# Kernel optimization log

Measured on AMD Instinct MI355X. Metric: run time of the kernel, lower is better.

## Reference

```python
import jax, jax.numpy as jnp
import numpy as np
from jax import lax

B, S, D = 4, 4096, 1024
EPS = 1e-6  # flax RMSNorm default epsilon


def setup_inputs() -> dict:
    key = jax.random.key(0)
    ks = jax.random.split(key, 8)
    std = 0.01  # flax.linen.initializers.normal() default stddev
    return {
        "x": jax.random.normal(ks[0], (B, S, D), dtype=jnp.float32),
        "wq": jax.random.normal(ks[1], (D, D), dtype=jnp.float32) * std,
        "wk": jax.random.normal(ks[2], (D, D), dtype=jnp.float32) * std,
        "wv": jax.random.normal(ks[3], (D, D), dtype=jnp.float32) * std,
        "wa": jax.random.normal(ks[4], (D, 2 * D), dtype=jnp.float32) * std,
        "wg": jax.random.normal(ks[5], (D, D), dtype=jnp.float32) * std,
        "wo": jax.random.normal(ks[6], (D, D), dtype=jnp.float32) * std,
        "rms_scale": jnp.ones((D,), dtype=jnp.float32),  # RMSNorm scale param
    }


def gate_loop_operator(k, v, q, a):
    # data-dependent complex linear recurrence: h_t = a_t * h_{t-1} + k_t * v_t
    def binary_operator(e_i, e_j):
        a_i, kv_i = e_i
        a_j, kv_j = e_j
        return (a_j * a_i, a_j * kv_i + kv_j)

    kv = (k * v).astype(jnp.complex64)
    _, y = lax.associative_scan(binary_operator, (a, kv), axis=1)
    return q * jnp.real(y)


def reference(x, wq, wk, wv, wa, wg, wo, rms_scale):
    # RMSNorm (flax default: no mean subtraction, learned scale)
    xn = x * lax.rsqrt(jnp.mean(x * x, axis=-1, keepdims=True) + EPS) * rms_scale

    q = xn @ wq
    k = xn @ wk
    v = xn @ wv
    a = xn @ wa  # [B, S, 2D]
    g = xn @ wg

    a_r, a_i = jnp.split(a, 2, axis=-1)
    a_c = lax.complex(a_r, a_i)
    magnitude = jax.nn.sigmoid(jnp.abs(a_c))  # constrain |a| < 1 for stability
    phase = jnp.angle(a_c)
    a_c = magnitude * jnp.exp(1j * phase)

    y = gate_loop_operator(k, v, q, a_c)
    y = y * jax.nn.silu(g)
    return y @ wo
```

## Files before the change

kernel.cpp:

```cpp
#include <hip/hip_runtime.h>
#include <hip/hip_bf16.h>
#include <math.h>

#define BDIM 4
#define SDIM 4096
#define DDIM 1024
#define MROWS (BDIM*SDIM)
#define EPS 1e-6f
#define NCHUNK 64
#define LCHUNK 64

typedef _Float16 f16_t;
typedef _Float16 f16x4_t __attribute__((ext_vector_type(4)));
typedef _Float16 f16x8_t __attribute__((ext_vector_type(8)));
typedef float    f32x4_t __attribute__((ext_vector_type(4)));

__device__ __forceinline__ void gload16(const void* g, void* l) {
    __builtin_amdgcn_global_load_lds(
        (const __attribute__((address_space(1))) unsigned int*)g,
        (__attribute__((address_space(3))) unsigned int*)l, 16, 0, 0);
}

__global__ __launch_bounds__(256) void fill_kernel(float* __restrict__ out,
                                                   int n, float val)
{
    const int i = blockIdx.x * 256 + threadIdx.x;
    if (i < n) out[i] = val;
}

__global__ __launch_bounds__(256) void rmsnorm_kernel(
    const float* __restrict__ x, const float* __restrict__ scale,
    f16_t* __restrict__ xn)
{
    const int row = blockIdx.x;
    const int tid = threadIdx.x;
    const float4 v = reinterpret_cast<const float4*>(x + (size_t)row * DDIM)[tid];
    float ss = v.x*v.x + v.y*v.y + v.z*v.z + v.w*v.w;
    #pragma unroll
    for (int off = 32; off > 0; off >>= 1)
        ss += __shfl_down(ss, off, 64);
    __shared__ float red[4];
    if ((tid & 63) == 0) red[tid >> 6] = ss;
    __syncthreads();
    ss = red[0] + red[1] + red[2] + red[3];
    const float inv = rsqrtf(ss * (1.0f / DDIM) + EPS);
    const float4 sc = reinterpret_cast<const float4*>(scale)[tid];
    f16x4_t o;
    o.x = (f16_t)(v.x * inv * sc.x);
    o.y = (f16_t)(v.y * inv * sc.y);
    o.z = (f16_t)(v.z * inv * sc.z);
    o.w = (f16_t)(v.w * inv * sc.w);
    reinterpret_cast<f16x4_t*>(xn + (size_t)row * DDIM)[tid] = o;
}

__global__ __launch_bounds__(256) void transpose_f16_kernel(
    const float* __restrict__ W, f16_t* __restrict__ WT, int K, int N)
{
    __shared__ float t[32][33];
    const int kb = blockIdx.y * 32;
    const int nb = blockIdx.x * 32;
    const int r  = threadIdx.x >> 3;
    const int c0 = (threadIdx.x & 7) << 2;
    const float4 v = *reinterpret_cast<const float4*>(&W[(size_t)(kb + r) * N + nb + c0]);
    t[r][c0 + 0] = v.x; t[r][c0 + 1] = v.y; t[r][c0 + 2] = v.z; t[r][c0 + 3] = v.w;
    __syncthreads();
    f16x4_t o;
    o.x = (f16_t)t[c0 + 0][r];
    o.y = (f16_t)t[c0 + 1][r];
    o.z = (f16_t)t[c0 + 2][r];
    o.w = (f16_t)t[c0 + 3][r];
    *reinterpret_cast<f16x4_t*>(&WT[(size_t)(nb + r) * K + kb + c0]) = o;
}

__global__ __launch_bounds__(256) void transpose_a_kernel(
    const float* __restrict__ W, f16_t* __restrict__ WT)
{
    const int K = DDIM, N = 2 * DDIM;
    __shared__ float t[32][33];
    const int kb = blockIdx.y * 32;
    const int nb = blockIdx.x * 32;
    const int r  = threadIdx.x >> 3;
    const int c0 = (threadIdx.x & 7) << 2;
    const int base = (c0 < 16) ? ((nb >> 1) + c0) : (DDIM + (nb >> 1) + c0 - 16);
    const float4 v = *reinterpret_cast<const float4*>(&W[(size_t)(kb + r) * N + base]);
    t[r][c0 + 0] = v.x; t[r][c0 + 1] = v.y; t[r][c0 + 2] = v.z; t[r][c0 + 3] = v.w;
    __syncthreads();
    const int rr  = threadIdx.x >> 3;
    const int cc0 = (threadIdx.x & 7) << 2;
    const int ctile = (rr >> 1) + (rr & 1) * 16;
    f16x4_t o;
    o.x = (f16_t)t[cc0 + 0][ctile];
    o.y = (f16_t)t[cc0 + 1][ctile];
    o.z = (f16_t)t[cc0 + 2][ctile];
    o.w = (f16_t)t[cc0 + 3][ctile];
    *reinterpret_cast<f16x4_t*>(&WT[(size_t)(nb + rr) * K + kb + cc0]) = o;
}

template <int MODE>
__global__ __launch_bounds__(256, 2) void mfma_gemm_kernel(
    const f16_t* __restrict__ A, const f16_t* __restrict__ BT,
    void* __restrict__ Cv, void* __restrict__ Cv2, void* __restrict__ Cv3,
    int M, int N, int K)
{
    __shared__ __align__(16) f16_t As[128 * 32];
    __shared__ __align__(16) f16_t Bs[128 * 32];

    const int tid  = threadIdx.x;
    const int wave = tid >> 6;
    const int lane = tid & 63;
    const int bm = blockIdx.y * 128;
    const int bn = blockIdx.x * 128;
    const int wm = (wave & 1) * 64;
    const int wn = (wave >> 1) * 64;

    const int sr = tid >> 2;
    const int sc = (tid & 3) * 8;
    const f16_t* Ag = A  + (size_t)(bm + sr) * K + sc;
    const f16_t* Bg = BT + (size_t)(bn + sr) * K + sc;
    f16_t* Al0 = As + tid * 8;
    f16_t* Al1 = As + 64 * 32 + tid * 8;
    f16_t* Bl0 = Bs + tid * 8;
    f16_t* Bl1 = Bs + 64 * 32 + tid * 8;
    const size_t rowskip = (size_t)64 * K;

    f32x4_t acc[4][4] = {};

    const int fm = lane & 15;
    const int kh = (lane >> 4) << 3;

    for (int kt = 0; kt < K; kt += 32) {
        gload16(Ag + kt, Al0);
        gload16(Ag + rowskip + kt, Al1);
        gload16(Bg + kt, Bl0);
        gload16(Bg + rowskip + kt, Bl1);
        __syncthreads();

        f16x8_t af[4], bfr[4];
        #pragma unroll
        for (int i = 0; i < 4; ++i)
            af[i] = *reinterpret_cast<const f16x8_t*>(&As[(wm + i * 16 + fm) * 32 + kh]);
        #pragma unroll
        for (int j = 0; j < 4; ++j)
            bfr[j] = *reinterpret_cast<const f16x8_t*>(&Bs[(wn + j * 16 + fm) * 32 + kh]);
        #pragma unroll
        for (int i = 0; i < 4; ++i)
            #pragma unroll
            for (int j = 0; j < 4; ++j)
                acc[i][j] = __builtin_amdgcn_mfma_f32_16x16x32_f16(
                    af[i], bfr[j], acc[i][j], 0, 0, 0);
        __syncthreads();
    }

    const int erow = (lane >> 4) << 2;
    const int ecol = lane & 15;
    #pragma unroll
    for (int i = 0; i < 4; ++i) {
        #pragma unroll
        for (int j = 0; j < 4; ++j) {
            const int row0 = bm + wm + i * 16 + erow;
            const int col  = bn + wn + j * 16 + ecol;
            #pragma unroll
            for (int rg = 0; rg < 4; ++rg) {
                const size_t idx = (size_t)(row0 + rg) * N + col;
                const float val = acc[i][j][rg];
                if (MODE == 0) {
                    ((float*)Cv)[idx] = val;
                } else if (MODE == 2) {
                    f16_t* C = (f16_t*)Cv;
                    C[idx] = (f16_t)((float)C[idx] * val);
                } else if (MODE == 4) {
                    const float par = __shfl_xor(val, 1, 64);
                    const float re = (lane & 1) ? par : val;
                    const float im = (lane & 1) ? val : par;
                    const float r = sqrtf(re * re + im * im);
                    float outv;
                    if (r > 0.0f) {
                        const float sg = 1.0f / (1.0f + expf(-r));
                        outv = val * (sg / r);
                    } else {
                        outv = (lane & 1) ? 0.0f : 0.5f;
                    }
                    ((float*)Cv)[idx] = outv;
                } else {
                    f16_t* dst = (bn < 1024) ? (f16_t*)Cv
                               : (bn < 2048) ? (f16_t*)Cv2 : (f16_t*)Cv3;
                    const size_t didx = (size_t)(row0 + rg) * DDIM + ((bn & 1023) + wn + j * 16 + ecol);
                    dst[didx] = (f16_t)val;
                }
            }
        }
    }
}

__global__ __launch_bounds__(256) void scan1_kernel(
    const float* __restrict__ a, const f16_t* __restrict__ kvb,
    float4* __restrict__ state)
{
    const int t = blockIdx.x * 256 + threadIdx.x;
    const int d = t & 1023;
    const int c = (t >> 10) & (NCHUNK - 1);
    const int b = t >> 16;
    size_t base  = ((size_t)(b * SDIM + c * LCHUNK)) * DDIM + d;
    const float2* a2 = (const float2*)a;
    float Ar = 1.0f, Ai = 0.0f, Hr = 0.0f, Hi = 0.0f;
    for (int s = 0; s < LCHUNK; ++s) {
        const float2 av = a2[base];
        const float kv = (float)kvb[base];
        const float hr = av.x * Hr - av.y * Hi + kv;
        const float hi = av.x * Hi + av.y * Hr;
        Hr = hr; Hi = hi;
        const float nr = av.x * Ar - av.y * Ai;
        const float ni = av.x * Ai + av.y * Ar;
        Ar = nr; Ai = ni;
        base += DDIM;
    }
    state[t] = make_float4(Ar, Ai, Hr, Hi);
}

__global__ __launch_bounds__(256) void scan2_kernel(
    const float4* __restrict__ state, float2* __restrict__ carry)
{
    const int t = blockIdx.x * 256 + threadIdx.x;
    const int d = t & 1023;
    const int b = t >> 10;
    float cr = 0.0f, ci = 0.0f;
    for (int c = 0; c < NCHUNK; ++c) {
        const size_t idx = ((size_t)(b * NCHUNK + c)) * DDIM + d;
        carry[idx] = make_float2(cr, ci);
        const float4 st = state[idx];
        const float nr = st.x * cr - st.y * ci + st.z;
        const float ni = st.x * ci + st.y * cr + st.w;
        cr = nr; ci = ni;
    }
}

__global__ __launch_bounds__(256) void scan3_kernel(
    const float* __restrict__ a, f16_t* __restrict__ kvb,
    const f16_t* __restrict__ qb, const f16_t* __restrict__ gb,
    const float2* __restrict__ carry)
{
    const int t = blockIdx.x * 256 + threadIdx.x;
    const int d = t & 1023;
    const int c = (t >> 10) & (NCHUNK - 1);
    const int b = t >> 16;
    size_t base  = ((size_t)(b * SDIM + c * LCHUNK)) * DDIM + d;
    const float2* a2 = (const float2*)a;
    const float2 h0 = carry[t];
    float Hr = h0.x, Hi = h0.y;
    for (int s = 0; s < LCHUNK; ++s) {
        const float2 av = a2[base];
        const float kv = (float)kvb[base];
        const float hr = av.x * Hr - av.y * Hi + kv;
        const float hi = av.x * Hi + av.y * Hr;
        Hr = hr; Hi = hi;
        const float qv = (float)qb[base];
        const float gv = (float)gb[base];
        const float silu = gv / (1.0f + expf(-gv));
        kvb[base] = (f16_t)(qv * silu * Hr);
        base += DDIM;
    }
}

extern "C" void kernel_launch(void* const* d_in, const int* in_sizes, int n_in,
                              void* d_out, int out_size, void* d_ws, size_t ws_size,
                              hipStream_t stream)
{
    const float* x        = (const float*)d_in[0];
    const float* wq       = (const float*)d_in[1];
    const float* wk       = (const float*)d_in[2];
    const float* wv       = (const float*)d_in[3];
    const float* wa       = (const float*)d_in[4];
    const float* wg       = (const float*)d_in[5];
    const float* wo       = (const float*)d_in[6];
    const float* rms_scale= (const float*)d_in[7];
    float* out = (float*)d_out;

    const size_t SZ = (size_t)MROWS * DDIM;
    const size_t WSZ = (size_t)DDIM * DDIM;
    char* ws = (char*)d_ws;
    f16_t* xn   = (f16_t*)ws;
    f16_t* kv   = (f16_t*)(ws + SZ * 2);
    float* abuf = (float*)(ws + SZ * 4);
    f16_t* WT   = (f16_t*)(ws + SZ * 12);
    f16_t* WTq = WT;
    f16_t* WTk = WT + WSZ;
    f16_t* WTg = WT + 2 * WSZ;
    f16_t* WTv = WT + 3 * WSZ;
    f16_t* WTa = WT + 4 * WSZ;
    f16_t* WTo = WT + 6 * WSZ;
    float4* state = (float4*)xn;
    float2* carry = (float2*)WT;

    f16_t* qb = (f16_t*)d_out;
    f16_t* gb = qb + SZ;

    const size_t needed = SZ * 12 + 7 * WSZ * 2;
    if (ws_size < needed) {
        const float marker = (float)(ws_size >> 20);
        fill_kernel<<<(out_size + 255) / 256, 256, 0, stream>>>(out, out_size, marker);
        return;
    }

    rmsnorm_kernel<<<MROWS, 256, 0, stream>>>(x, rms_scale, xn);

    dim3 tblk(256);
    dim3 tg1(DDIM / 32, DDIM / 32);
    transpose_f16_kernel<<<tg1, tblk, 0, stream>>>(wq, WTq, DDIM, DDIM);
    transpose_f16_kernel<<<tg1, tblk, 0, stream>>>(wk, WTk, DDIM, DDIM);
    transpose_f16_kernel<<<tg1, tblk, 0, stream>>>(wg, WTg, DDIM, DDIM);
    transpose_f16_kernel<<<tg1, tblk, 0, stream>>>(wv, WTv, DDIM, DDIM);
    transpose_f16_kernel<<<tg1, tblk, 0, stream>>>(wo, WTo, DDIM, DDIM);
    dim3 tga(2 * DDIM / 32, DDIM / 32);
    transpose_a_kernel<<<tga, tblk, 0, stream>>>(wa, WTa);

    dim3 blk(256);
    dim3 gqkg(3 * DDIM / 128, MROWS / 128);
    dim3 g1(DDIM / 128, MROWS / 128);
    dim3 g2(2 * DDIM / 128, MROWS / 128);
    mfma_gemm_kernel<5><<<gqkg, blk, 0, stream>>>(xn, WT,  qb, kv, gb, MROWS, 3 * DDIM, DDIM);
    mfma_gemm_kernel<2><<<g1,   blk, 0, stream>>>(xn, WTv, kv, nullptr, nullptr, MROWS, DDIM, DDIM);
    mfma_gemm_kernel<4><<<g2,   blk, 0, stream>>>(xn, WTa, abuf, nullptr, nullptr, MROWS, 2 * DDIM, DDIM);

    const int nscan = BDIM * NCHUNK * DDIM;
    scan1_kernel<<<nscan / 256, 256, 0, stream>>>(abuf, kv, state);
    scan2_kernel<<<(BDIM * DDIM) / 256, 256, 0, stream>>>(state, carry);
    scan3_kernel<<<nscan / 256, 256, 0, stream>>>(abuf, kv, qb, gb, carry);

    mfma_gemm_kernel<0><<<g1, blk, 0, stream>>>(kv, WTo, out, nullptr, nullptr, MROWS, DDIM, DDIM);
}
```

Baseline: 591.3 us.

## Store gate coefficients in fp16, parallelize carry scan, merge weight transposes

```diff
diff --git a/kernel.cpp b/kernel.cpp
--- a/kernel.cpp
+++ b/kernel.cpp
@@ -11,6 +11,7 @@
 #define LCHUNK 64
 
 typedef _Float16 f16_t;
+typedef _Float16 f16x2_t __attribute__((ext_vector_type(2)));
 typedef _Float16 f16x4_t __attribute__((ext_vector_type(4)));
 typedef _Float16 f16x8_t __attribute__((ext_vector_type(8)));
 typedef float    f32x4_t __attribute__((ext_vector_type(4)));
@@ -53,9 +54,17 @@
     reinterpret_cast<f16x4_t*>(xn + (size_t)row * DDIM)[tid] = o;
 }
 
-__global__ __launch_bounds__(256) void transpose_f16_kernel(
-    const float* __restrict__ W, f16_t* __restrict__ WT, int K, int N)
-{
+__global__ __launch_bounds__(256) void transpose5_kernel(
+    const float* __restrict__ w0, const float* __restrict__ w1,
+    const float* __restrict__ w2, const float* __restrict__ w3,
+    const float* __restrict__ w4, f16_t* __restrict__ WT)
+{
+    const int K = DDIM, N = DDIM;
+    const int z = blockIdx.z;
+    const float* W = (z == 0) ? w0 : (z == 1) ? w1 : (z == 2) ? w2
+                   : (z == 3) ? w3 : w4;
+    const int zoff = (z == 4) ? 6 : z;
+    f16_t* dst = WT + (size_t)zoff * DDIM * DDIM;
     __shared__ float t[32][33];
     const int kb = blockIdx.y * 32;
     const int nb = blockIdx.x * 32;
@@ -69,7 +78,7 @@
     o.y = (f16_t)t[c0 + 1][r];
     o.z = (f16_t)t[c0 + 2][r];
     o.w = (f16_t)t[c0 + 3][r];
-    *reinterpret_cast<f16x4_t*>(&WT[(size_t)(nb + r) * K + kb + c0]) = o;
+    *reinterpret_cast<f16x4_t*>(&dst[(size_t)(nb + r) * K + kb + c0]) = o;
 }
 
 __global__ __launch_bounds__(256) void transpose_a_kernel(
@@ -175,12 +184,12 @@
                     const float r = sqrtf(re * re + im * im);
                     float outv;
                     if (r > 0.0f) {
-                        const float sg = 1.0f / (1.0f + expf(-r));
+                        const float sg = 1.0f / (1.0f + __expf(-r));
                         outv = val * (sg / r);
                     } else {
                         outv = (lane & 1) ? 0.0f : 0.5f;
                     }
-                    ((float*)Cv)[idx] = outv;
+                    ((f16_t*)Cv)[idx] = (f16_t)outv;
                 } else {
                     f16_t* dst = (bn < 1024) ? (f16_t*)Cv
                                : (bn < 2048) ? (f16_t*)Cv2 : (f16_t*)Cv3;
@@ -193,7 +202,7 @@
 }
 
 __global__ __launch_bounds__(256) void scan1_kernel(
-    const float* __restrict__ a, const f16_t* __restrict__ kvb,
+    const f16x2_t* __restrict__ a2, const f16_t* __restrict__ kvb,
     float4* __restrict__ state)
 {
     const int t = blockIdx.x * 256 + threadIdx.x;
@@ -201,16 +210,17 @@
     const int c = (t >> 10) & (NCHUNK - 1);
     const int b = t >> 16;
     size_t base  = ((size_t)(b * SDIM + c * LCHUNK)) * DDIM + d;
-    const float2* a2 = (const float2*)a;
     float Ar = 1.0f, Ai = 0.0f, Hr = 0.0f, Hi = 0.0f;
     for (int s = 0; s < LCHUNK; ++s) {
-        const float2 av = a2[base];
+        const f16x2_t av = a2[base];
+        const float arr = (float)av.x;
+        const float aii = (float)av.y;
         const float kv = (float)kvb[base];
-        const float hr = av.x * Hr - av.y * Hi + kv;
-        const float hi = av.x * Hi + av.y * Hr;
+        const float hr = arr * Hr - aii * Hi + kv;
+        const float hi = arr * Hi + aii * Hr;
         Hr = hr; Hi = hi;
-        const float nr = av.x * Ar - av.y * Ai;
-        const float ni = av.x * Ai + av.y * Ar;
+        const float nr = arr * Ar - aii * Ai;
+        const float ni = arr * Ai + aii * Ar;
         Ar = nr; Ai = ni;
         base += DDIM;
     }
@@ -221,21 +231,34 @@
     const float4* __restrict__ state, float2* __restrict__ carry)
 {
     const int t = blockIdx.x * 256 + threadIdx.x;
-    const int d = t & 1023;
-    const int b = t >> 10;
-    float cr = 0.0f, ci = 0.0f;
-    for (int c = 0; c < NCHUNK; ++c) {
-        const size_t idx = ((size_t)(b * NCHUNK + c)) * DDIM + d;
-        carry[idx] = make_float2(cr, ci);
-        const float4 st = state[idx];
-        const float nr = st.x * cr - st.y * ci + st.z;
-        const float ni = st.x * ci + st.y * cr + st.w;
-        cr = nr; ci = ni;
-    }
+    const int c = t & 63;
+    const int ch = t >> 6;
+    const int d = ch & 1023;
+    const int b = ch >> 10;
+    const size_t idx = ((size_t)(b * NCHUNK + c)) * DDIM + d;
+    const float4 st = state[idx];
+    float Ar = st.x, Ai = st.y, Hr = st.z, Hi = st.w;
+    #pragma unroll
+    for (int off = 1; off < 64; off <<= 1) {
+        const float pAr = __shfl_up(Ar, off, 64);
+        const float pAi = __shfl_up(Ai, off, 64);
+        const float pHr = __shfl_up(Hr, off, 64);
+        const float pHi = __shfl_up(Hi, off, 64);
+        if (c >= off) {
+            const float nHr = Ar * pHr - Ai * pHi + Hr;
+            const float nHi = Ar * pHi + Ai * pHr + Hi;
+            const float nAr = Ar * pAr - Ai * pAi;
+            const float nAi = Ar * pAi + Ai * pAr;
+            Ar = nAr; Ai = nAi; Hr = nHr; Hi = nHi;
+        }
+    }
+    const float eHr = __shfl_up(Hr, 1, 64);
+    const float eHi = __shfl_up(Hi, 1, 64);
+    carry[idx] = make_float2(c == 0 ? 0.0f : eHr, c == 0 ? 0.0f : eHi);
 }
 
 __global__ __launch_bounds__(256) void scan3_kernel(
-    const float* __restrict__ a, f16_t* __restrict__ kvb,
+    const f16x2_t* __restrict__ a2, f16_t* __restrict__ kvb,
     const f16_t* __restrict__ qb, const f16_t* __restrict__ gb,
     const float2* __restrict__ carry)
 {
@@ -244,18 +267,19 @@
     const int c = (t >> 10) & (NCHUNK - 1);
     const int b = t >> 16;
     size_t base  = ((size_t)(b * SDIM + c * LCHUNK)) * DDIM + d;
-    const float2* a2 = (const float2*)a;
     const float2 h0 = carry[t];
     float Hr = h0.x, Hi = h0.y;
     for (int s = 0; s < LCHUNK; ++s) {
-        const float2 av = a2[base];
+        const f16x2_t av = a2[base];
+        const float arr = (float)av.x;
+        const float aii = (float)av.y;
         const float kv = (float)kvb[base];
-        const float hr = av.x * Hr - av.y * Hi + kv;
-        const float hi = av.x * Hi + av.y * Hr;
+        const float hr = arr * Hr - aii * Hi + kv;
+        const float hi = arr * Hi + aii * Hr;
         Hr = hr; Hi = hi;
         const float qv = (float)qb[base];
         const float gv = (float)gb[base];
-        const float silu = gv / (1.0f + expf(-gv));
+        const float silu = gv / (1.0f + __expf(-gv));
         kvb[base] = (f16_t)(qv * silu * Hr);
         base += DDIM;
     }
@@ -278,13 +302,10 @@
     const size_t SZ = (size_t)MROWS * DDIM;
     const size_t WSZ = (size_t)DDIM * DDIM;
     char* ws = (char*)d_ws;
-    f16_t* xn   = (f16_t*)ws;
-    f16_t* kv   = (f16_t*)(ws + SZ * 2);
-    float* abuf = (float*)(ws + SZ * 4);
-    f16_t* WT   = (f16_t*)(ws + SZ * 12);
-    f16_t* WTq = WT;
-    f16_t* WTk = WT + WSZ;
-    f16_t* WTg = WT + 2 * WSZ;
+    f16_t*   xn   = (f16_t*)ws;
+    f16_t*   kv   = (f16_t*)(ws + SZ * 2);
+    f16x2_t* abuf = (f16x2_t*)(ws + SZ * 4);
+    f16_t*   WT   = (f16_t*)(ws + SZ * 8);
     f16_t* WTv = WT + 3 * WSZ;
     f16_t* WTa = WT + 4 * WSZ;
     f16_t* WTo = WT + 6 * WSZ;
@@ -294,7 +315,7 @@
     f16_t* qb = (f16_t*)d_out;
     f16_t* gb = qb + SZ;
 
-    const size_t needed = SZ * 12 + 7 * WSZ * 2;
+    const size_t needed = SZ * 8 + 7 * WSZ * 2;
     if (ws_size < needed) {
         const float marker = (float)(ws_size >> 20);
         fill_kernel<<<(out_size + 255) / 256, 256, 0, stream>>>(out, out_size, marker);
@@ -304,12 +325,8 @@
     rmsnorm_kernel<<<MROWS, 256, 0, stream>>>(x, rms_scale, xn);
 
     dim3 tblk(256);
-    dim3 tg1(DDIM / 32, DDIM / 32);
-    transpose_f16_kernel<<<tg1, tblk, 0, stream>>>(wq, WTq, DDIM, DDIM);
-    transpose_f16_kernel<<<tg1, tblk, 0, stream>>>(wk, WTk, DDIM, DDIM);
-    transpose_f16_kernel<<<tg1, tblk, 0, stream>>>(wg, WTg, DDIM, DDIM);
-    transpose_f16_kernel<<<tg1, tblk, 0, stream>>>(wv, WTv, DDIM, DDIM);
-    transpose_f16_kernel<<<tg1, tblk, 0, stream>>>(wo, WTo, DDIM, DDIM);
+    dim3 tg5(DDIM / 32, DDIM / 32, 5);
+    transpose5_kernel<<<tg5, tblk, 0, stream>>>(wq, wk, wg, wv, wo, WT);
     dim3 tga(2 * DDIM / 32, DDIM / 32);
     transpose_a_kernel<<<tga, tblk, 0, stream>>>(wa, WTa);
 
@@ -323,7 +340,7 @@
 
     const int nscan = BDIM * NCHUNK * DDIM;
     scan1_kernel<<<nscan / 256, 256, 0, stream>>>(abuf, kv, state);
-    scan2_kernel<<<(BDIM * DDIM) / 256, 256, 0, stream>>>(state, carry);
+    scan2_kernel<<<nscan / 256, 256, 0, stream>>>(state, carry);
     scan3_kernel<<<nscan / 256, 256, 0, stream>>>(abuf, kv, qb, gb, carry);
 
     mfma_gemm_kernel<0><<<g1, blk, 0, stream>>>(kv, WTo, out, nullptr, nullptr, MROWS, DDIM, DDIM);
```

Result: faster. 552.0 us (-6.6%).
